# Kernel optimization log

Measured on AMD Instinct MI355X. Metric: run time of the kernel, lower is better.

Reference implementation:

```python
import jax, jax.numpy as jnp
import numpy as np

N, E = 20000, 320000
IN_DIM = 18            # 2 (pos) + k_feat=16
P = 32                 # in_proj_out
H1, D1 = 8, 32         # gat1 heads, head_dim (out_dim = P*heads = 256)
OUT = P * H1           # 256
BD, H2, D2 = 256, 8, 32  # bottleneck dim / heads / head_dim
NID = 1000             # num_real_ids
NEG_SLOPE = 0.2


def _ln(x, g, b, eps=1e-5):
    mu = x.mean(-1, keepdims=True)
    v = ((x - mu) ** 2).mean(-1, keepdims=True)
    return (x - mu) * jax.lax.rsqrt(v + eps) * g + b


def _segment_softmax(score, dst, n):
    # score: [E, H], softmax over edges sharing the same dst node
    m = jax.ops.segment_max(score, dst, num_segments=n)
    e = jnp.exp(score - m[dst])
    s = jax.ops.segment_sum(e, dst, num_segments=n)
    return e / (s[dst] + 1e-16)


def _gatv2(x, src, dst, ea, Wl, Wr, We, att, bias, n, h, d):
    # GATv2 (PyG semantics): e_ij = att . leaky_relu(Wl x_j + Wr x_i + We e_ij)
    xl = (x @ Wl).reshape(n, h, d)           # source transform
    xr = (x @ Wr).reshape(n, h, d)           # target transform
    xe = (ea @ We).reshape(-1, h, d)         # edge embedding [E,h,d]
    f = jax.nn.leaky_relu(xl[src] + xr[dst] + xe, NEG_SLOPE)  # [E,h,d]
    score = jnp.einsum('ehd,hd->eh', f, att)                   # [E,h]
    alpha = _segment_softmax(score, dst, n)                    # [E,h]
    out = jax.ops.segment_sum(alpha[:, :, None] * xl[src], dst, num_segments=n)
    return out.reshape(n, h * d) + bias


def setup_inputs() -> dict:
    key = jax.random.key(0)
    ks = jax.random.split(key, 20)
    s = 0.05
    rn = lambda k, shape: (jax.random.normal(k, shape, jnp.float32) * s)
    return {
        'x_gnn': jax.random.normal(ks[0], (N, IN_DIM), jnp.float32),
        'edge_index': jax.random.randint(ks[1], (2, E), 0, N),
        'edge_attr': jax.random.uniform(ks[2], (E, 1), dtype=jnp.float32),
        'W_in': rn(ks[3], (IN_DIM, P)), 'b_in': jnp.zeros((P,), jnp.float32),
        'Wl1': rn(ks[4], (P, OUT)), 'Wr1': rn(ks[5], (P, OUT)),
        'We1': rn(ks[6], (1, OUT)), 'att1': rn(ks[7], (H1, D1)),
        'bg1': jnp.zeros((OUT,), jnp.float32),
        'ln1_g': jnp.ones((OUT,), jnp.float32), 'ln1_b': jnp.zeros((OUT,), jnp.float32),
        'W_down': rn(ks[8], (OUT, BD)),
        'lnd_g': jnp.ones((BD,), jnp.float32), 'lnd_b': jnp.zeros((BD,), jnp.float32),
        'Wl2': rn(ks[9], (BD, BD)), 'Wr2': rn(ks[10], (BD, BD)),
        'We2': rn(ks[11], (1, BD)), 'att2': rn(ks[12], (H2, D2)),
        'bg2': jnp.zeros((BD,), jnp.float32),
        'ln2_g': jnp.ones((BD,), jnp.float32), 'ln2_b': jnp.zeros((BD,), jnp.float32),
        'W_up': rn(ks[13], (BD, OUT)),
        'lnu_g': jnp.ones((OUT,), jnp.float32), 'lnu_b': jnp.zeros((OUT,), jnp.float32),
        'W_cls': rn(ks[14], (OUT, NID)), 'b_cls': jnp.zeros((NID,), jnp.float32),
    }


def reference(x_gnn, edge_index, edge_attr, W_in, b_in,
              Wl1, Wr1, We1, att1, bg1, ln1_g, ln1_b,
              W_down, lnd_g, lnd_b,
              Wl2, Wr2, We2, att2, bg2, ln2_g, ln2_b,
              W_up, lnu_g, lnu_b, W_cls, b_cls):
    src, dst = edge_index[0], edge_index[1]
    h0 = x_gnn @ W_in + b_in
    # GATv2Block 1: conv + LN (no residual, 32 -> 256)
    g1 = _gatv2(h0, src, dst, edge_attr, Wl1, Wr1, We1, att1, bg1, N, H1, D1)
    h1 = _ln(g1, ln1_g, ln1_b)
    # bottleneck branch
    z = _ln(h1 @ W_down, lnd_g, lnd_b)
    # GATv2Block 2: conv + residual + LN (256 -> 256)
    g2 = _gatv2(z, src, dst, edge_attr, Wl2, Wr2, We2, att2, bg2, N, H2, D2)
    z2 = _ln(g2 + z, ln2_g, ln2_b)
    h2 = z2 @ W_up                       # up projection (dropout is identity in eval)
    h = _ln(h1 + h2, lnu_g, lnu_b)
    logits = h @ W_cls + b_cls
    return (logits, h)
```

## Files before the change

### kernel.cpp

```cpp
#include <hip/hip_runtime.h>
#include <math.h>

#define N_NODES 20000
#define N_EDGES 320000

typedef __attribute__((ext_vector_type(8))) __bf16 bf16x8;
typedef __attribute__((ext_vector_type(8))) unsigned short ushort8;
typedef __attribute__((ext_vector_type(4))) float floatx4;

__device__ __forceinline__ unsigned short f2b(float f) {
    unsigned int u = __float_as_uint(f);
    unsigned int r = (u + 0x7fffu + ((u >> 16) & 1u)) >> 16;
    return (unsigned short)r;
}
__device__ __forceinline__ float b2f(unsigned short u) {
    return __uint_as_float(((unsigned int)u) << 16);
}

__global__ void k_inproj(const float* __restrict__ x, const float* __restrict__ W,
                         const float* __restrict__ b, unsigned short* __restrict__ h0) {
    int t = blockIdx.x * blockDim.x + threadIdx.x;
    if (t >= N_NODES * 32) return;
    int n = t >> 5, p = t & 31;
    float acc = b[p];
    const float* xr = x + n * 18;
#pragma unroll
    for (int k = 0; k < 18; k++) acc = fmaf(xr[k], W[k * 32 + p], acc);
    h0[t] = f2b(acc);
}

__global__ void k_wcvt_all(const float* __restrict__ Wl1, const float* __restrict__ Wr1,
                           const float* __restrict__ Wdn, const float* __restrict__ Wl2,
                           const float* __restrict__ Wr2, const float* __restrict__ Wup,
                           const float* __restrict__ Wcl,
                           unsigned short* __restrict__ o1, unsigned short* __restrict__ o2,
                           unsigned short* __restrict__ o3, unsigned short* __restrict__ o4,
                           unsigned short* __restrict__ o5, unsigned short* __restrict__ o6,
                           unsigned short* __restrict__ o7) {
    int t = blockIdx.x * blockDim.x + threadIdx.x;
    const float* W; unsigned short* O; int Nd, K, idx; bool swz;
    if (t < 8192)        { W = Wl1; O = o1; Nd = 256;  K = 32;  idx = t;          swz = false; }
    else if (t < 16384)  { W = Wr1; O = o2; Nd = 256;  K = 32;  idx = t - 8192;   swz = false; }
    else if (t < 81920)  { W = Wdn; O = o3; Nd = 256;  K = 256; idx = t - 16384;  swz = true; }
    else if (t < 147456) { W = Wl2; O = o4; Nd = 256;  K = 256; idx = t - 81920;  swz = true; }
    else if (t < 212992) { W = Wr2; O = o5; Nd = 256;  K = 256; idx = t - 147456; swz = true; }
    else if (t < 278528) { W = Wup; O = o6; Nd = 256;  K = 256; idx = t - 212992; swz = true; }
    else if (t < 540672) { W = Wcl; O = o7; Nd = 1000; K = 256; idx = t - 278528; swz = true; }
    else return;
    int n = idx / K, k = idx % K;
    float v = (n < Nd) ? W[(size_t)k * Nd + n] : 0.f;
    int pos = swz ? (n * K + ((((k >> 3) ^ (n & 7)) << 3) | (k & 7))) : idx;
    O[pos] = f2b(v);
}

__global__ __launch_bounds__(256) void k_gemm_bf16(
    const unsigned short* __restrict__ A, const unsigned short* __restrict__ Bt,
    float* __restrict__ Cf, unsigned short* __restrict__ Cb,
    const float* __restrict__ bias, int M, int N, int K) {
    __shared__ unsigned short As[8 * 64 * 8];
    __shared__ unsigned short Bs[8 * 64 * 8];
    int tid = threadIdx.x;
    int wave = tid >> 6, lane = tid & 63;
    int wr = wave >> 1, wc = wave & 1;
    int row0 = blockIdx.x * 128, col0 = blockIdx.y * 128;
    floatx4 zero4 = {0.f, 0.f, 0.f, 0.f};
    floatx4 acc[4][4];
#pragma unroll
    for (int i = 0; i < 4; i++)
#pragma unroll
        for (int j = 0; j < 4; j++) acc[i][j] = zero4;
    for (int kb = 0; kb < K; kb += 32) {
#pragma unroll
        for (int q = 0; q < 2; q++) {
            int c = tid * 2 + q;
            int row = c >> 2, koff = (c & 3) * 8;
            int lp = (row & 15) + 16 * (koff >> 3);
            int mt = row >> 4;
            ushort8 va = {0, 0, 0, 0, 0, 0, 0, 0};
            if (row0 + row < M)
                va = *(const ushort8*)(A + (size_t)(row0 + row) * K + kb + koff);
            *(ushort8*)(As + (mt * 64 + lp) * 8) = va;
            ushort8 vb = {0, 0, 0, 0, 0, 0, 0, 0};
            if (col0 + row < N)
                vb = *(const ushort8*)(Bt + (size_t)(col0 + row) * K + kb + koff);
            *(ushort8*)(Bs + (mt * 64 + lp) * 8) = vb;
        }
        __syncthreads();
        bf16x8 af[4], bfr[4];
#pragma unroll
        for (int i = 0; i < 4; i++)
            af[i] = *(const bf16x8*)(As + ((wr * 4 + i) * 64 + lane) * 8);
#pragma unroll
        for (int j = 0; j < 4; j++)
            bfr[j] = *(const bf16x8*)(Bs + ((wc * 4 + j) * 64 + lane) * 8);
#pragma unroll
        for (int i = 0; i < 4; i++)
#pragma unroll
            for (int j = 0; j < 4; j++)
                acc[i][j] = __builtin_amdgcn_mfma_f32_16x16x32_bf16(
                    af[i], bfr[j], acc[i][j], 0, 0, 0);
        __syncthreads();
    }
    int quad = lane >> 4, nl = lane & 15;
#pragma unroll
    for (int i = 0; i < 4; i++) {
#pragma unroll
        for (int j = 0; j < 4; j++) {
            int col = col0 + wc * 64 + j * 16 + nl;
            if (col >= N) continue;
            float bv = bias ? bias[col] : 0.f;
#pragma unroll
            for (int r = 0; r < 4; r++) {
                int rr = row0 + wr * 64 + i * 16 + quad * 4 + r;
                if (rr >= M) continue;
                float v = acc[i][j][r] + bv;
                if (Cf) Cf[(size_t)rr * N + col] = v;
                else Cb[(size_t)rr * N + col] = f2b(v);
            }
        }
    }
}

__global__ __launch_bounds__(1024, 1) void k_gemm_ln(
    const unsigned short* __restrict__ A,
    const unsigned short* __restrict__ Bsw,
    int M, int Ncols, int ldC,
    const float* __restrict__ bias,
    const float* __restrict__ res,
    const float* __restrict__ g, const float* __restrict__ b,
    float* __restrict__ outf, unsigned short* __restrict__ outb) {
    __shared__ unsigned short Bs[256 * 256];
    __shared__ float red[4][64][2];
    int tid = threadIdx.x, lane = tid & 63, wave = tid >> 6;
    int wr = wave >> 2, wc = wave & 3;
    int nl = lane & 15, quad = lane >> 4;
    int row0 = blockIdx.x * 64, col0 = blockIdx.y * 256;

    const unsigned short* aptr =
        A + (size_t)(row0 + wr * 16 + nl) * 256 + quad * 8;
    bf16x8 a_cur, a_nxt;
    a_cur = *(const bf16x8*)(aptr);
    a_nxt = a_cur;

    {
        const ushort8* bsrc8 = (const ushort8*)(Bsw + (size_t)col0 * 256);
        ushort8* bdst8 = (ushort8*)Bs;
#pragma unroll
        for (int t = 0; t < 8; t++) bdst8[t * 1024 + tid] = bsrc8[t * 1024 + tid];
    }
    __syncthreads();

    floatx4 zero4 = {0.f, 0.f, 0.f, 0.f};
    floatx4 acc[4];
#pragma unroll
    for (int j = 0; j < 4; j++) acc[j] = zero4;

    int swx = nl & 7;
#pragma unroll
    for (int kb = 0; kb < 8; kb++) {
        if (kb < 7) a_nxt = *(const bf16x8*)(aptr + (kb + 1) * 32);
        int kq = kb * 4 + quad;
#pragma unroll
        for (int j = 0; j < 4; j++) {
            int c = wc * 64 + j * 16 + nl;
            bf16x8 bf = *(const bf16x8*)((const char*)Bs +
                                         (size_t)c * 512 + ((kq ^ swx) << 4));
            acc[j] = __builtin_amdgcn_mfma_f32_16x16x32_bf16(a_cur, bf, acc[j], 0, 0, 0);
        }
        a_cur = a_nxt;
    }

    if (g == nullptr) {
#pragma unroll
        for (int j = 0; j < 4; j++) {
            int col = col0 + wc * 64 + j * 16 + nl;
            if (col >= Ncols) continue;
            float bv = bias ? bias[col] : 0.f;
#pragma unroll
            for (int r = 0; r < 4; r++) {
                int rr = row0 + wr * 16 + quad * 4 + r;
                if (rr >= M) continue;
                float v = acc[j][r] + bv;
                if (outf) outf[(size_t)rr * ldC + col] = v;
                if (outb) outb[(size_t)rr * ldC + col] = f2b(v);
            }
        }
        return;
    }

    if (res) {
#pragma unroll
        for (int j = 0; j < 4; j++) {
            int col = wc * 64 + j * 16 + nl;
#pragma unroll
            for (int r = 0; r < 4; r++) {
                int rr = row0 + wr * 16 + quad * 4 + r;
                acc[j][r] += res[(size_t)rr * 256 + col];
            }
        }
    }
#pragma unroll
    for (int r = 0; r < 4; r++) {
        float s = 0.f, q = 0.f;
#pragma unroll
        for (int j = 0; j < 4; j++) {
            float v = acc[j][r];
            s += v;
            q = fmaf(v, v, q);
        }
        s += __shfl_xor(s, 1, 64); q += __shfl_xor(q, 1, 64);
        s += __shfl_xor(s, 2, 64); q += __shfl_xor(q, 2, 64);
        s += __shfl_xor(s, 4, 64); q += __shfl_xor(q, 4, 64);
        s += __shfl_xor(s, 8, 64); q += __shfl_xor(q, 8, 64);
        if (nl == 0) {
            int lr = wr * 16 + quad * 4 + r;
            red[wc][lr][0] = s;
            red[wc][lr][1] = q;
        }
    }
    __syncthreads();
    float mean_[4], rstd_[4];
#pragma unroll
    for (int r = 0; r < 4; r++) {
        int lr = wr * 16 + quad * 4 + r;
        float sum = red[0][lr][0] + red[1][lr][0] + red[2][lr][0] + red[3][lr][0];
        float sq  = red[0][lr][1] + red[1][lr][1] + red[2][lr][1] + red[3][lr][1];
        float mean = sum * (1.0f / 256.0f);
        float var = sq * (1.0f / 256.0f) - mean * mean;
        mean_[r] = mean;
        rstd_[r] = 1.0f / sqrtf(var + 1e-5f);
    }
#pragma unroll
    for (int j = 0; j < 4; j++) {
        int col = wc * 64 + j * 16 + nl;
        float gv = g[col], bvv = b[col];
#pragma unroll
        for (int r = 0; r < 4; r++) {
            int rr = row0 + wr * 16 + quad * 4 + r;
            if (rr >= M) continue;
            float o = (acc[j][r] - mean_[r]) * rstd_[r] * gv + bvv;
            if (outf) outf[(size_t)rr * 256 + col] = o;
            if (outb) outb[(size_t)rr * 256 + col] = f2b(o);
        }
    }
}

__global__ void k_hist(const int* __restrict__ dst, int* __restrict__ cnt) {
    int e = blockIdx.x * blockDim.x + threadIdx.x;
    if (e >= N_EDGES) return;
    atomicAdd(cnt + dst[e], 1);
}

__global__ __launch_bounds__(1024) void k_scan(const int* __restrict__ cnt,
                                               int* __restrict__ rowptr,
                                               int* __restrict__ wp, int n) {
    __shared__ int tsum[1024];
    int t = threadIdx.x;
    const int chunk = 20;
    int i0 = t * chunk;
    int local[chunk];
    int s = 0;
#pragma unroll
    for (int j = 0; j < chunk; j++) {
        int i = i0 + j;
        int v = (i < n) ? cnt[i] : 0;
        local[j] = s;
        s += v;
    }
    tsum[t] = s;
    __syncthreads();
    for (int off = 1; off < 1024; off <<= 1) {
        int other = (t >= off) ? tsum[t - off] : 0;
        __syncthreads();
        tsum[t] += other;
        __syncthreads();
    }
    int base = (t > 0) ? tsum[t - 1] : 0;
#pragma unroll
    for (int j = 0; j < chunk; j++) {
        int i = i0 + j;
        if (i < n) {
            int ex = base + local[j];
            rowptr[i] = ex;
            wp[i] = ex;
        }
    }
    if (t == 1023) rowptr[n] = tsum[1023];
}

__global__ void k_fill(const int* __restrict__ src, const int* __restrict__ dst,
                       const float* __restrict__ ea, int* __restrict__ wp,
                       int* __restrict__ srcs, float* __restrict__ eas) {
    int e = blockIdx.x * blockDim.x + threadIdx.x;
    if (e >= N_EDGES) return;
    int p = atomicAdd(wp + dst[e], 1);
    srcs[p] = src[e];
    eas[p] = ea[e];
}

__global__ __launch_bounds__(256) void k_gat_ln(
    const int* __restrict__ rowptr, const int* __restrict__ srcs,
    const float* __restrict__ eas, const unsigned short* __restrict__ xlr,
    const float* __restrict__ We, const float* __restrict__ att,
    const float* __restrict__ vbias, const float* __restrict__ res,
    const float* __restrict__ g, const float* __restrict__ b,
    float* __restrict__ outf, unsigned short* __restrict__ outb) {
    int node = blockIdx.x * 4 + (threadIdx.x >> 6);
    if (node >= N_NODES) return;
    int lane = threadIdx.x & 63;
    int beg = rowptr[node], end = rowptr[node + 1];
    float4 wv = ((const float4*)We)[lane];
    float4 av = ((const float4*)att)[lane];
    ushort4 xru = ((const ushort4*)(xlr + (size_t)node * 512 + 256))[lane];
    float4 rv = make_float4(b2f(xru.x), b2f(xru.y), b2f(xru.z), b2f(xru.w));
    float m = -3.0e38f, l = 0.f;
    float4 acc = make_float4(0.f, 0.f, 0.f, 0.f);
    if (beg < end) {
        int last = end - 1;
        int i1 = (beg + 1 < end) ? beg + 1 : last;
        int i2 = (beg + 2 < end) ? beg + 2 : last;
        int i3 = (beg + 3 < end) ? beg + 3 : last;
        int i4 = (beg + 4 < end) ? beg + 4 : last;
        int i5 = (beg + 5 < end) ? beg + 5 : last;
        int i6 = (beg + 6 < end) ? beg + 6 : last;
        int i7 = (beg + 7 < end) ? beg + 7 : last;
        int s0a = srcs[beg], s0b = srcs[i1];
        int s1a = srcs[i2],  s1b = srcs[i3];
        int s2a = srcs[i4],  s2b = srcs[i5];
        int s3a = srcs[i6],  s3b = srcs[i7];
        float a0a = eas[beg], a0b = eas[i1];
        float a1a = eas[i2],  a1b = eas[i3];
        float a2a = eas[i4],  a2b = eas[i5];
        float a3a = eas[i6],  a3b = eas[i7];
        ushort4 x0a = ((const ushort4*)(xlr + (size_t)s0a * 512))[lane];
        ushort4 x0b = ((const ushort4*)(xlr + (size_t)s0b * 512))[lane];
        ushort4 x1a = ((const ushort4*)(xlr + (size_t)s1a * 512))[lane];
        ushort4 x1b = ((const ushort4*)(xlr + (size_t)s1b * 512))[lane];
        ushort4 x2a = ((const ushort4*)(xlr + (size_t)s2a * 512))[lane];
        ushort4 x2b = ((const ushort4*)(xlr + (size_t)s2b * 512))[lane];
        for (int i = beg; i < end; i += 2) {
            int j8 = (i + 8 < end) ? i + 8 : last;
            int j9 = (i + 9 < end) ? i + 9 : last;
            int s4a = srcs[j8], s4b = srcs[j9];
            float a4a = eas[j8], a4b = eas[j9];
            ushort4 x3a = ((const ushort4*)(xlr + (size_t)s3a * 512))[lane];
            ushort4 x3b = ((const ushort4*)(xlr + (size_t)s3b * 512))[lane];
            float4 lva = make_float4(b2f(x0a.x), b2f(x0a.y), b2f(x0a.z), b2f(x0a.w));
            float4 lvb = make_float4(b2f(x0b.x), b2f(x0b.y), b2f(x0b.z), b2f(x0b.w));
            float f, pa = 0.f, pb = 0.f;
            f = lva.x + rv.x + a0a * wv.x; f = fmaxf(f, 0.2f * f); pa = fmaf(f, av.x, pa);
            f = lva.y + rv.y + a0a * wv.y; f = fmaxf(f, 0.2f * f); pa = fmaf(f, av.y, pa);
            f = lva.z + rv.z + a0a * wv.z; f = fmaxf(f, 0.2f * f); pa = fmaf(f, av.z, pa);
            f = lva.w + rv.w + a0a * wv.w; f = fmaxf(f, 0.2f * f); pa = fmaf(f, av.w, pa);
            f = lvb.x + rv.x + a0b * wv.x; f = fmaxf(f, 0.2f * f); pb = fmaf(f, av.x, pb);
            f = lvb.y + rv.y + a0b * wv.y; f = fmaxf(f, 0.2f * f); pb = fmaf(f, av.y, pb);
            f = lvb.z + rv.z + a0b * wv.z; f = fmaxf(f, 0.2f * f); pb = fmaf(f, av.z, pb);
            f = lvb.w + rv.w + a0b * wv.w; f = fmaxf(f, 0.2f * f); pb = fmaf(f, av.w, pb);
            pa += __shfl_xor(pa, 1, 64);
            pa += __shfl_xor(pa, 2, 64);
            pa += __shfl_xor(pa, 4, 64);
            pb += __shfl_xor(pb, 1, 64);
            pb += __shfl_xor(pb, 2, 64);
            pb += __shfl_xor(pb, 4, 64);
            if (i + 1 >= end) pb = -3.0e38f;
            float mnew = fmaxf(fmaxf(m, pa), pb);
            float scale = __expf(m - mnew);
            float wa = __expf(pa - mnew);
            float wb = __expf(pb - mnew);
            acc.x = fmaf(acc.x, scale, fmaf(wa, lva.x, wb * lvb.x));
            acc.y = fmaf(acc.y, scale, fmaf(wa, lva.y, wb * lvb.y));
            acc.z = fmaf(acc.z, scale, fmaf(wa, lva.z, wb * lvb.z));
            acc.w = fmaf(acc.w, scale, fmaf(wa, lva.w, wb * lvb.w));
            l = fmaf(l, scale, wa + wb);
            m = mnew;
            x0a = x1a; x0b = x1b; x1a = x2a; x1b = x2b; x2a = x3a; x2b = x3b;
            a0a = a1a; a0b = a1b; a1a = a2a; a1b = a2b; a2a = a3a; a2b = a3b;
            a3a = a4a; a3b = a4b; s3a = s4a; s3b = s4b;
        }
    }
    float inv = 1.0f / (l + 1e-16f);
    float4 vb4 = ((const float4*)vbias)[lane];
    float4 o = make_float4(fmaf(acc.x, inv, vb4.x), fmaf(acc.y, inv, vb4.y),
                           fmaf(acc.z, inv, vb4.z), fmaf(acc.w, inv, vb4.w));
    if (res) {
        float4 r4 = ((const float4*)(res + (size_t)node * 256))[lane];
        o.x += r4.x; o.y += r4.y; o.z += r4.z; o.w += r4.w;
    }
    float sum = o.x + o.y + o.z + o.w;
#pragma unroll
    for (int off = 32; off > 0; off >>= 1) sum += __shfl_xor(sum, off, 64);
    float mean = sum * (1.0f / 256.0f);
    float dx = o.x - mean, dy = o.y - mean, dz = o.z - mean, dw = o.w - mean;
    float sq = dx * dx + dy * dy + dz * dz + dw * dw;
#pragma unroll
    for (int off = 32; off > 0; off >>= 1) sq += __shfl_xor(sq, off, 64);
    float rstd = 1.0f / sqrtf(sq * (1.0f / 256.0f) + 1e-5f);
    float4 gg = ((const float4*)g)[lane];
    float4 bb = ((const float4*)b)[lane];
    float4 o4 = make_float4(dx * rstd * gg.x + bb.x, dy * rstd * gg.y + bb.y,
                            dz * rstd * gg.z + bb.z, dw * rstd * gg.w + bb.w);
    if (outf) ((float4*)(outf + (size_t)node * 256))[lane] = o4;
    if (outb) {
        ushort4 u;
        u.x = f2b(o4.x); u.y = f2b(o4.y); u.z = f2b(o4.z); u.w = f2b(o4.w);
        ((ushort4*)(outb + (size_t)node * 256))[lane] = u;
    }
}

extern "C" void kernel_launch(void* const* d_in, const int* in_sizes, int n_in,
                              void* d_out, int out_size, void* d_ws, size_t ws_size,
                              hipStream_t stream) {
    const float* x_gnn = (const float*)d_in[0];
    const int* ei = (const int*)d_in[1];
    const int* src = ei;
    const int* dst = ei + N_EDGES;
    const float* ea   = (const float*)d_in[2];
    const float* W_in = (const float*)d_in[3];
    const float* b_in = (const float*)d_in[4];
    const float* Wl1  = (const float*)d_in[5];
    const float* Wr1  = (const float*)d_in[6];
    const float* We1  = (const float*)d_in[7];
    const float* att1 = (const float*)d_in[8];
    const float* bg1  = (const float*)d_in[9];
    const float* ln1_g = (const float*)d_in[10];
    const float* ln1_b = (const float*)d_in[11];
    const float* W_down = (const float*)d_in[12];
    const float* lnd_g = (const float*)d_in[13];
    const float* lnd_b = (const float*)d_in[14];
    const float* Wl2  = (const float*)d_in[15];
    const float* Wr2  = (const float*)d_in[16];
    const float* We2  = (const float*)d_in[17];
    const float* att2 = (const float*)d_in[18];
    const float* bg2  = (const float*)d_in[19];
    const float* ln2_g = (const float*)d_in[20];
    const float* ln2_b = (const float*)d_in[21];
    const float* W_up = (const float*)d_in[22];
    const float* lnu_g = (const float*)d_in[23];
    const float* lnu_b = (const float*)d_in[24];
    const float* W_cls = (const float*)d_in[25];
    const float* b_cls = (const float*)d_in[26];

    float* ws = (float*)d_ws;
    float* B_agg = ws;
    float* B_h1  = B_agg + 5120000;
    float* B_z   = B_h1 + 5120000;
    unsigned short* B_xlr = (unsigned short*)(B_z + 5120000);
    unsigned short* B_actb = B_xlr + 10240000;
    unsigned short* B_h0b = B_actb + 5120000;
    unsigned short* Wt_l1 = B_h0b + 640000;
    unsigned short* Wt_r1 = Wt_l1 + 8192;
    unsigned short* Wt_down = Wt_r1 + 8192;
    unsigned short* Wt_l2 = Wt_down + 65536;
    unsigned short* Wt_r2 = Wt_l2 + 65536;
    unsigned short* Wt_up = Wt_r2 + 65536;
    unsigned short* Wt_cls = Wt_up + 65536;
    int* C_cnt = (int*)(Wt_cls + 262144);
    int* C_row = C_cnt + 20000;
    int* C_wp  = C_row + 20001;
    int* C_src = C_wp + 20000;
    float* C_ea = (float*)(C_src + 320000);

    float* out_logits = (float*)d_out;
    float* out_h = out_logits + (size_t)N_NODES * 1000;

    int gatblk = (N_NODES + 3) / 4;
    int gemmM64 = (N_NODES + 63) / 64;
    dim3 gl((N_NODES + 127) / 128, 4);

    hipMemsetAsync(C_cnt, 0, (size_t)20000 * 4, stream);
    k_hist<<<(N_EDGES + 255) / 256, 256, 0, stream>>>(dst, C_cnt);
    k_scan<<<1, 1024, 0, stream>>>(C_cnt, C_row, C_wp, N_NODES);
    k_fill<<<(N_EDGES + 255) / 256, 256, 0, stream>>>(src, dst, ea, C_wp, C_src, C_ea);

    k_wcvt_all<<<(540672 + 255) / 256, 256, 0, stream>>>(
        Wl1, Wr1, W_down, Wl2, Wr2, W_up, W_cls,
        Wt_l1, Wt_r1, Wt_down, Wt_l2, Wt_r2, Wt_up, Wt_cls);

    k_inproj<<<(N_NODES * 32 + 255) / 256, 256, 0, stream>>>(x_gnn, W_in, b_in, B_h0b);
    k_gemm_bf16<<<gl, 256, 0, stream>>>(B_h0b, Wt_l1, nullptr, B_xlr, nullptr, N_NODES, 512, 32);
    k_gat_ln<<<gatblk, 256, 0, stream>>>(C_row, C_src, C_ea, B_xlr, We1, att1,
                                         bg1, nullptr, ln1_g, ln1_b, B_h1, B_actb);
    k_gemm_ln<<<dim3(gemmM64, 1), 1024, 0, stream>>>(
        B_actb, Wt_down, N_NODES, 256, 256, nullptr, nullptr, lnd_g, lnd_b, B_z, B_actb);
    k_gemm_ln<<<dim3(gemmM64, 2), 1024, 0, stream>>>(
        B_actb, Wt_l2, N_NODES, 512, 512, nullptr, nullptr, nullptr, nullptr, nullptr, B_xlr);
    k_gat_ln<<<gatblk, 256, 0, stream>>>(C_row, C_src, C_ea, B_xlr, We2, att2,
                                         bg2, B_z, ln2_g, ln2_b, nullptr, B_actb);
    k_gemm_ln<<<dim3(gemmM64, 1), 1024, 0, stream>>>(
        B_actb, Wt_up, N_NODES, 256, 256, nullptr, B_h1, lnu_g, lnu_b, out_h, B_actb);
    k_gemm_ln<<<dim3(gemmM64, 4), 1024, 0, stream>>>(
        B_actb, Wt_cls, N_NODES, 1000, 1000, b_cls, nullptr, nullptr, nullptr,
        out_logits, nullptr);
}
```

Before: 430.1 us.

## Hold GEMM weights in registers with small row tiles and fuse prep kernels

The 1024-thread LDS-staged GEMM+LayerNorm kernel becomes a 512-thread kernel over 16-row tiles. Each wave keeps its 32-column weight slice in registers, and only the A tile is staged in swizzled shared memory. The separate in-projection, histogram and weight-conversion kernels are merged into one launch, and the weight swizzle is dropped because weights are now read directly from global memory. The aim is to remove the 128KB LDS fill per block, raise occupancy and cut launch count, at the cost of reloading weights from L2 in every block and more register pressure.

```diff
diff --git a/kernel.cpp b/kernel.cpp
--- a/kernel.cpp
+++ b/kernel.cpp
@@ -17,40 +17,44 @@
     return __uint_as_float(((unsigned int)u) << 16);
 }
 
-__global__ void k_inproj(const float* __restrict__ x, const float* __restrict__ W,
-                         const float* __restrict__ b, unsigned short* __restrict__ h0) {
+__global__ void k_prep(const float* __restrict__ x, const float* __restrict__ Wi,
+                       const float* __restrict__ bi, unsigned short* __restrict__ h0,
+                       const int* __restrict__ dst, int* __restrict__ cnt,
+                       const float* __restrict__ Wl1, const float* __restrict__ Wr1,
+                       const float* __restrict__ Wdn, const float* __restrict__ Wl2,
+                       const float* __restrict__ Wr2, const float* __restrict__ Wup,
+                       const float* __restrict__ Wcl,
+                       unsigned short* __restrict__ o1, unsigned short* __restrict__ o2,
+                       unsigned short* __restrict__ o3, unsigned short* __restrict__ o4,
+                       unsigned short* __restrict__ o5, unsigned short* __restrict__ o6,
+                       unsigned short* __restrict__ o7) {
     int t = blockIdx.x * blockDim.x + threadIdx.x;
-    if (t >= N_NODES * 32) return;
-    int n = t >> 5, p = t & 31;
-    float acc = b[p];
-    const float* xr = x + n * 18;
-#pragma unroll
-    for (int k = 0; k < 18; k++) acc = fmaf(xr[k], W[k * 32 + p], acc);
-    h0[t] = f2b(acc);
-}
-
-__global__ void k_wcvt_all(const float* __restrict__ Wl1, const float* __restrict__ Wr1,
-                           const float* __restrict__ Wdn, const float* __restrict__ Wl2,
-                           const float* __restrict__ Wr2, const float* __restrict__ Wup,
-                           const float* __restrict__ Wcl,
-                           unsigned short* __restrict__ o1, unsigned short* __restrict__ o2,
-                           unsigned short* __restrict__ o3, unsigned short* __restrict__ o4,
-                           unsigned short* __restrict__ o5, unsigned short* __restrict__ o6,
-                           unsigned short* __restrict__ o7) {
-    int t = blockIdx.x * blockDim.x + threadIdx.x;
-    const float* W; unsigned short* O; int Nd, K, idx; bool swz;
-    if (t < 8192)        { W = Wl1; O = o1; Nd = 256;  K = 32;  idx = t;          swz = false; }
-    else if (t < 16384)  { W = Wr1; O = o2; Nd = 256;  K = 32;  idx = t - 8192;   swz = false; }
-    else if (t < 81920)  { W = Wdn; O = o3; Nd = 256;  K = 256; idx = t - 16384;  swz = true; }
-    else if (t < 147456) { W = Wl2; O = o4; Nd = 256;  K = 256; idx = t - 81920;  swz = true; }
-    else if (t < 212992) { W = Wr2; O = o5; Nd = 256;  K = 256; idx = t - 147456; swz = true; }
-    else if (t < 278528) { W = Wup; O = o6; Nd = 256;  K = 256; idx = t - 212992; swz = true; }
-    else if (t < 540672) { W = Wcl; O = o7; Nd = 1000; K = 256; idx = t - 278528; swz = true; }
+    if (t < 640000) {
+        int n = t >> 5, p = t & 31;
+        float acc = bi[p];
+        const float* xr = x + n * 18;
+#pragma unroll
+        for (int k = 0; k < 18; k++) acc = fmaf(xr[k], Wi[k * 32 + p], acc);
+        h0[t] = f2b(acc);
+        return;
+    }
+    if (t < 960000) {
+        atomicAdd(cnt + dst[t - 640000], 1);
+        return;
+    }
+    int u = t - 960000;
+    const float* W; unsigned short* O; int Nd, K, idx;
+    if (u < 8192)        { W = Wl1; O = o1; Nd = 256;  K = 32;  idx = u; }
+    else if (u < 16384)  { W = Wr1; O = o2; Nd = 256;  K = 32;  idx = u - 8192; }
+    else if (u < 81920)  { W = Wdn; O = o3; Nd = 256;  K = 256; idx = u - 16384; }
+    else if (u < 147456) { W = Wl2; O = o4; Nd = 256;  K = 256; idx = u - 81920; }
+    else if (u < 212992) { W = Wr2; O = o5; Nd = 256;  K = 256; idx = u - 147456; }
+    else if (u < 278528) { W = Wup; O = o6; Nd = 256;  K = 256; idx = u - 212992; }
+    else if (u < 540672) { W = Wcl; O = o7; Nd = 1000; K = 256; idx = u - 278528; }
     else return;
     int n = idx / K, k = idx % K;
     float v = (n < Nd) ? W[(size_t)k * Nd + n] : 0.f;
-    int pos = swz ? (n * K + ((((k >> 3) ^ (n & 7)) << 3) | (k & 7))) : idx;
-    O[pos] = f2b(v);
+    O[idx] = f2b(v);
 }
 
 __global__ __launch_bounds__(256) void k_gemm_bf16(
@@ -121,65 +125,55 @@
     }
 }
 
-__global__ __launch_bounds__(1024, 1) void k_gemm_ln(
+__global__ __launch_bounds__(512) void k_gemm_reg(
     const unsigned short* __restrict__ A,
-    const unsigned short* __restrict__ Bsw,
-    int M, int Ncols, int ldC,
+    const unsigned short* __restrict__ Bt,
+    int Ncols, int ldC,
     const float* __restrict__ bias,
     const float* __restrict__ res,
     const float* __restrict__ g, const float* __restrict__ b,
     float* __restrict__ outf, unsigned short* __restrict__ outb) {
-    __shared__ unsigned short Bs[256 * 256];
-    __shared__ float red[4][64][2];
+    __shared__ unsigned short As[16 * 256];
+    __shared__ float red[8][16][2];
     int tid = threadIdx.x, lane = tid & 63, wave = tid >> 6;
-    int wr = wave >> 2, wc = wave & 3;
     int nl = lane & 15, quad = lane >> 4;
-    int row0 = blockIdx.x * 64, col0 = blockIdx.y * 256;
-
-    const unsigned short* aptr =
-        A + (size_t)(row0 + wr * 16 + nl) * 256 + quad * 8;
-    bf16x8 a_cur, a_nxt;
-    a_cur = *(const bf16x8*)(aptr);
-    a_nxt = a_cur;
+    int row0 = blockIdx.x * 16;
+    int cbase = blockIdx.y * 256 + wave * 32;
 
     {
-        const ushort8* bsrc8 = (const ushort8*)(Bsw + (size_t)col0 * 256);
-        ushort8* bdst8 = (ushort8*)Bs;
-#pragma unroll
-        for (int t = 0; t < 8; t++) bdst8[t * 1024 + tid] = bsrc8[t * 1024 + tid];
-    }
+        int r = tid >> 5, c = tid & 31;
+        ushort8 v = *(const ushort8*)(A + (size_t)(row0 + r) * 256 + c * 8);
+        *(ushort8*)(As + r * 256 + ((c ^ (r & 7)) << 3)) = v;
+    }
+    bf16x8 breg[2][8];
+    const unsigned short* bptr = Bt + (size_t)(cbase + nl) * 256 + quad * 8;
+#pragma unroll
+    for (int j = 0; j < 2; j++)
+#pragma unroll
+        for (int kb = 0; kb < 8; kb++)
+            breg[j][kb] = *(const bf16x8*)(bptr + j * 16 * 256 + kb * 32);
     __syncthreads();
 
     floatx4 zero4 = {0.f, 0.f, 0.f, 0.f};
-    floatx4 acc[4];
-#pragma unroll
-    for (int j = 0; j < 4; j++) acc[j] = zero4;
-
-    int swx = nl & 7;
+    floatx4 acc[2];
+    acc[0] = zero4; acc[1] = zero4;
 #pragma unroll
     for (int kb = 0; kb < 8; kb++) {
-        if (kb < 7) a_nxt = *(const bf16x8*)(aptr + (kb + 1) * 32);
         int kq = kb * 4 + quad;
-#pragma unroll
-        for (int j = 0; j < 4; j++) {
-            int c = wc * 64 + j * 16 + nl;
-            bf16x8 bf = *(const bf16x8*)((const char*)Bs +
-                                         (size_t)c * 512 + ((kq ^ swx) << 4));
-            acc[j] = __builtin_amdgcn_mfma_f32_16x16x32_bf16(a_cur, bf, acc[j], 0, 0, 0);
-        }
-        a_cur = a_nxt;
+        bf16x8 a = *(const bf16x8*)(As + nl * 256 + (((kq ^ (nl & 7))) << 3));
+        acc[0] = __builtin_amdgcn_mfma_f32_16x16x32_bf16(a, breg[0][kb], acc[0], 0, 0, 0);
+        acc[1] = __builtin_amdgcn_mfma_f32_16x16x32_bf16(a, breg[1][kb], acc[1], 0, 0, 0);
     }
 
     if (g == nullptr) {
 #pragma unroll
-        for (int j = 0; j < 4; j++) {
-            int col = col0 + wc * 64 + j * 16 + nl;
+        for (int j = 0; j < 2; j++) {
+            int col = cbase + j * 16 + nl;
             if (col >= Ncols) continue;
             float bv = bias ? bias[col] : 0.f;
 #pragma unroll
             for (int r = 0; r < 4; r++) {
-                int rr = row0 + wr * 16 + quad * 4 + r;
-                if (rr >= M) continue;
+                int rr = row0 + quad * 4 + r;
                 float v = acc[j][r] + bv;
                 if (outf) outf[(size_t)rr * ldC + col] = v;
                 if (outb) outb[(size_t)rr * ldC + col] = f2b(v);
@@ -190,65 +184,51 @@
 
     if (res) {
 #pragma unroll
-        for (int j = 0; j < 4; j++) {
-            int col = wc * 64 + j * 16 + nl;
-#pragma unroll
-            for (int r = 0; r < 4; r++) {
-                int rr = row0 + wr * 16 + quad * 4 + r;
-                acc[j][r] += res[(size_t)rr * 256 + col];
-            }
+        for (int j = 0; j < 2; j++) {
+            int col = cbase + j * 16 + nl;
+#pragma unroll
+            for (int r = 0; r < 4; r++)
+                acc[j][r] += res[(size_t)(row0 + quad * 4 + r) * 256 + col];
         }
     }
 #pragma unroll
     for (int r = 0; r < 4; r++) {
-        float s = 0.f, q = 0.f;
-#pragma unroll
-        for (int j = 0; j < 4; j++) {
-            float v = acc[j][r];
-            s += v;
-            q = fmaf(v, v, q);
-        }
+        float s = acc[0][r] + acc[1][r];
+        float q = fmaf(acc[0][r], acc[0][r], acc[1][r] * acc[1][r]);
         s += __shfl_xor(s, 1, 64); q += __shfl_xor(q, 1, 64);
         s += __shfl_xor(s, 2, 64); q += __shfl_xor(q, 2, 64);
         s += __shfl_xor(s, 4, 64); q += __shfl_xor(q, 4, 64);
         s += __shfl_xor(s, 8, 64); q += __shfl_xor(q, 8, 64);
         if (nl == 0) {
-            int lr = wr * 16 + quad * 4 + r;
-            red[wc][lr][0] = s;
-            red[wc][lr][1] = q;
+            red[wave][quad * 4 + r][0] = s;
+            red[wave][quad * 4 + r][1] = q;
         }
     }
     __syncthreads();
     float mean_[4], rstd_[4];
 #pragma unroll
     for (int r = 0; r < 4; r++) {
-        int lr = wr * 16 + quad * 4 + r;
-        float sum = red[0][lr][0] + red[1][lr][0] + red[2][lr][0] + red[3][lr][0];
-        float sq  = red[0][lr][1] + red[1][lr][1] + red[2][lr][1] + red[3][lr][1];
-        float mean = sum * (1.0f / 256.0f);
-        float var = sq * (1.0f / 256.0f) - mean * mean;
+        int row = quad * 4 + r;
+        float s = 0.f, q = 0.f;
+#pragma unroll
+        for (int w = 0; w < 8; w++) { s += red[w][row][0]; q += red[w][row][1]; }
+        float mean = s * (1.0f / 256.0f);
+        float var = q * (1.0f / 256.0f) - mean * mean;
         mean_[r] = mean;
         rstd_[r] = 1.0f / sqrtf(var + 1e-5f);
     }
 #pragma unroll
-    for (int j = 0; j < 4; j++) {
-        int col = wc * 64 + j * 16 + nl;
+    for (int j = 0; j < 2; j++) {
+        int col = cbase + j * 16 + nl;
         float gv = g[col], bvv = b[col];
 #pragma unroll
         for (int r = 0; r < 4; r++) {
-            int rr = row0 + wr * 16 + quad * 4 + r;
-            if (rr >= M) continue;
+            int rr = row0 + quad * 4 + r;
             float o = (acc[j][r] - mean_[r]) * rstd_[r] * gv + bvv;
             if (outf) outf[(size_t)rr * 256 + col] = o;
             if (outb) outb[(size_t)rr * 256 + col] = f2b(o);
         }
     }
-}
-
-__global__ void k_hist(const int* __restrict__ dst, int* __restrict__ cnt) {
-    int e = blockIdx.x * blockDim.x + threadIdx.x;
-    if (e >= N_EDGES) return;
-    atomicAdd(cnt + dst[e], 1);
 }
 
 __global__ __launch_bounds__(1024) void k_scan(const int* __restrict__ cnt,
@@ -464,31 +444,28 @@
     float* out_h = out_logits + (size_t)N_NODES * 1000;
 
     int gatblk = (N_NODES + 3) / 4;
-    int gemmM64 = (N_NODES + 63) / 64;
+    int gemmM16 = N_NODES / 16;
     dim3 gl((N_NODES + 127) / 128, 4);
 
     hipMemsetAsync(C_cnt, 0, (size_t)20000 * 4, stream);
-    k_hist<<<(N_EDGES + 255) / 256, 256, 0, stream>>>(dst, C_cnt);
+    k_prep<<<5862, 256, 0, stream>>>(x_gnn, W_in, b_in, B_h0b, dst, C_cnt,
+                                     Wl1, Wr1, W_down, Wl2, Wr2, W_up, W_cls,
+                                     Wt_l1, Wt_r1, Wt_down, Wt_l2, Wt_r2, Wt_up, Wt_cls);
     k_scan<<<1, 1024, 0, stream>>>(C_cnt, C_row, C_wp, N_NODES);
     k_fill<<<(N_EDGES + 255) / 256, 256, 0, stream>>>(src, dst, ea, C_wp, C_src, C_ea);
 
-    k_wcvt_all<<<(540672 + 255) / 256, 256, 0, stream>>>(
-        Wl1, Wr1, W_down, Wl2, Wr2, W_up, W_cls,
-        Wt_l1, Wt_r1, Wt_down, Wt_l2, Wt_r2, Wt_up, Wt_cls);
-
-    k_inproj<<<(N_NODES * 32 + 255) / 256, 256, 0, stream>>>(x_gnn, W_in, b_in, B_h0b);
     k_gemm_bf16<<<gl, 256, 0, stream>>>(B_h0b, Wt_l1, nullptr, B_xlr, nullptr, N_NODES, 512, 32);
     k_gat_ln<<<gatblk, 256, 0, stream>>>(C_row, C_src, C_ea, B_xlr, We1, att1,
                                          bg1, nullptr, ln1_g, ln1_b, B_h1, B_actb);
-    k_gemm_ln<<<dim3(gemmM64, 1), 1024, 0, stream>>>(
-        B_actb, Wt_down, N_NODES, 256, 256, nullptr, nullptr, lnd_g, lnd_b, B_z, B_actb);
-    k_gemm_ln<<<dim3(gemmM64, 2), 1024, 0, stream>>>(
-        B_actb, Wt_l2, N_NODES, 512, 512, nullptr, nullptr, nullptr, nullptr, nullptr, B_xlr);
+    k_gemm_reg<<<dim3(gemmM16, 1), 512, 0, stream>>>(
+        B_actb, Wt_down, 256, 256, nullptr, nullptr, lnd_g, lnd_b, B_z, B_actb);
+    k_gemm_reg<<<dim3(gemmM16, 2), 512, 0, stream>>>(
+        B_actb, Wt_l2, 512, 512, nullptr, nullptr, nullptr, nullptr, nullptr, B_xlr);
     k_gat_ln<<<gatblk, 256, 0, stream>>>(C_row, C_src, C_ea, B_xlr, We2, att2,
                                          bg2, B_z, ln2_g, ln2_b, nullptr, B_actb);
-    k_gemm_ln<<<dim3(gemmM64, 1), 1024, 0, stream>>>(
-        B_actb, Wt_up, N_NODES, 256, 256, nullptr, B_h1, lnu_g, lnu_b, out_h, B_actb);
-    k_gemm_ln<<<dim3(gemmM64, 4), 1024, 0, stream>>>(
-        B_actb, Wt_cls, N_NODES, 1000, 1000, b_cls, nullptr, nullptr, nullptr,
+    k_gemm_reg<<<dim3(gemmM16, 1), 512, 0, stream>>>(
+        B_actb, Wt_up, 256, 256, nullptr, B_h1, lnu_g, lnu_b, out_h, B_actb);
+    k_gemm_reg<<<dim3(gemmM16, 4), 512, 0, stream>>>(
+        B_actb, Wt_cls, 1000, 1000, b_cls, nullptr, nullptr, nullptr,
         out_logits, nullptr);
 }
```

Measured after the change: 478.2 us. 1.11x slower.
